# Performance work log

Measured on AMD Instinct MI355X. Metric: run time of the kernel, lower is better.

Reference implementation:

```python
import jax, jax.numpy as jnp
import numpy as np

SR = 22050
N_FFT = 16384
HOP = N_FFT // 2
NF = N_FFT // 2               # 8192 freq bins kept (last rfft bin dropped via [:-1])
H = SR / N_FFT                # uniform FFT-bin spacing in Hz
CENT = (440.0 * 2.0 ** ((np.arange(24, 108, 0.01) - 69.0) / 12.0)).astype(np.float32)  # [8400]
WIN = (0.5 - 0.5 * np.cos(2.0 * np.pi * np.arange(N_FFT) / N_FFT)).astype(np.float32)  # periodic hann

# Data-independent Thomas-algorithm coefficients for the not-a-knot cubic-spline
# tridiagonal system (diag=4, off-diags=1) with M_UNK unknowns (M_2..M_{n-3}).
M_UNK = NF - 4
_cp = np.empty(M_UNK); _inv_den = np.empty(M_UNK)
_inv_den[0] = 0.25; _cp[0] = 0.25
for _i in range(1, M_UNK):
    _inv_den[_i] = 1.0 / (4.0 - _cp[_i - 1])
    _cp[_i] = _inv_den[_i] if _i < M_UNK - 1 else 0.0
CP = jnp.asarray(_cp, jnp.float32)
INV_DEN = jnp.asarray(_inv_den, jnp.float32)
A_LOWER = jnp.asarray(np.where(np.arange(M_UNK) == 0, 0.0, 1.0), jnp.float32)


def _tridiag_solve(rhs):
    # Thomas algorithm with precomputed (data-independent) elimination coeffs.
    def fwd(dprev, xs):
        r, a, inv = xs
        dp = (r - a * dprev) * inv
        return dp, dp
    _, dp = jax.lax.scan(fwd, jnp.float32(0.0), (rhs, A_LOWER, INV_DEN))
    def bwd(xnext, xs):
        d_i, c_i = xs
        x = d_i - c_i * xnext
        return x, x
    _, xs = jax.lax.scan(bwd, jnp.float32(0.0), (dp, CP), reverse=True)
    return xs


def _cubic_interp(y, xq):
    # Not-a-knot cubic spline (scipy interp1d kind='cubic') on uniform grid x_i = i*H.
    h = jnp.float32(H)
    d = (y[:-2] - 2.0 * y[1:-1] + y[2:]) / (h * h)   # second-difference targets d_1..d_{n-2}
    M1, Mn2 = d[0], d[-1]                             # not-a-knot => M_1=d_1, M_{n-2}=d_{n-2}
    rhs = 6.0 * d[1:-1]
    rhs = rhs.at[0].add(-M1).at[-1].add(-Mn2)
    Min = _tridiag_solve(rhs)                         # M_2..M_{n-3}
    M = jnp.concatenate([jnp.stack([2.0 * M1 - Min[0], M1]), Min,
                         jnp.stack([Mn2, 2.0 * Mn2 - Min[-1]])])  # [n] second derivatives
    i = jnp.clip(jnp.floor(xq / h).astype(jnp.int32), 0, y.shape[0] - 2)
    t = xq - i.astype(jnp.float32) * h
    u = h - t
    Mi, Mi1, yi, yi1 = M[i], M[i + 1], y[i], y[i + 1]
    return ((Mi * u ** 3 + Mi1 * t ** 3) / (6.0 * h)
            + (yi - Mi * h * h / 6.0) * u / h
            + (yi1 - Mi1 * h * h / 6.0) * t / h)


def _tuning_scores(audio, w_smooth, w_detect):
    # torchaudio Spectrogram: center reflect-pad, periodic hann, power=2
    x = jnp.pad(audio, N_FFT // 2, mode='reflect')
    T = 1 + (x.shape[0] - N_FFT) // HOP
    idx = jnp.arange(T)[:, None] * HOP + jnp.arange(N_FFT)[None, :]
    frames = x[idx] * jnp.asarray(WIN)                 # [T, n_fft]
    spec = jnp.abs(jnp.fft.rfft(frames, axis=1)) ** 2  # [T, n_fft//2+1]
    fft_spec = jnp.log(100.0 * spec + 1.0).sum(0)[:NF] # sum over time, drop Nyquist bin
    cent = _cubic_interp(fft_spec, jnp.asarray(CENT))  # [8400]
    smoothed = jnp.convolve(cent, w_smooth, mode='same')
    filtered = jax.nn.relu(cent - smoothed)
    scores = jax.lax.conv_general_dilated(
        filtered[None, None, :], w_detect[None, None, :],
        window_strides=(1,), padding=[(50, 50)], rhs_dilation=(100,))[0, 0, :100]
    return scores


def setup_inputs():
    key = jax.random.key(0)
    audio = jax.random.normal(key, (16777216,), dtype=jnp.float32)
    w_smooth = jnp.ones((101,), jnp.float32) / 101.0   # mean filter, as in module init
    w_detect = jnp.ones((84,), jnp.float32)            # all-ones detector kernel
    return {"audio": audio, "w_smooth": w_smooth, "w_detect": w_detect}


def reference(audio, w_smooth, w_detect):
    scores = _tuning_scores(audio, w_smooth, w_detect)
    detuning = (jnp.argmax(scores) - 50).astype(jnp.int32)
    return detuning, scores
```

## Files before the change

### kernel.cpp

```cpp
#include <hip/hip_runtime.h>
#include <math.h>

#define NBINS   8192
#define L_AUDIO 16777216
#define T_FRAMES 2049
#define NQ      8400
#define MUNK    8188

__device__ __forceinline__ int refl_idx(int m) {
    if (m < 0) m = -m;
    if (m >= L_AUDIO) m = 2 * L_AUDIO - 2 - m;
    return m;
}
__device__ __forceinline__ float2 cmul(float2 a, float2 b) {
    return make_float2(fmaf(a.x, b.x, -a.y * b.y), fmaf(a.x, b.y, a.y * b.x));
}
__device__ __forceinline__ float2 csq(float2 a) {
    return make_float2(fmaf(a.x, a.x, -a.y * a.y), 2.0f * a.x * a.y);
}
__device__ __forceinline__ void r4(float2& x0, float2& x1, float2& x2, float2& x3,
                                   float2 w1, float2 w2, float2 w3) {
    float2 t0 = make_float2(x0.x + x2.x, x0.y + x2.y);
    float2 t1 = make_float2(x1.x + x3.x, x1.y + x3.y);
    float2 t2 = make_float2(x0.x - x2.x, x0.y - x2.y);
    float2 t3 = make_float2(x1.x - x3.x, x1.y - x3.y);
    float2 b1 = make_float2(t2.x + t3.y, t2.y - t3.x);
    float2 b3 = make_float2(t2.x - t3.y, t2.y + t3.x);
    x0 = make_float2(t0.x + t1.x, t0.y + t1.y);
    x1 = cmul(w1, b1);
    x2 = cmul(w2, make_float2(t0.x - t1.x, t0.y - t1.y));
    x3 = cmul(w3, b3);
}
__device__ __forceinline__ void r8(float2 x[8], float2 w) {
    const float c = 0.70710678118654752f;
    float2 w2 = csq(w), w3 = cmul(w, w2), w4 = csq(w2);
    r4(x[0], x[2], x[4], x[6], w, w2, w3);
    float2 wE   = make_float2(c * (w.x + w.y),  c * (w.y - w.x));
    float2 w2E2 = make_float2(w2.y, -w2.x);
    float2 w3E3 = make_float2(c * (w3.y - w3.x), -c * (w3.x + w3.y));
    r4(x[1], x[3], x[5], x[7], wE, w2E2, w3E3);
#pragma unroll
    for (int r = 0; r < 4; ++r) {
        float2 a = x[2 * r], b = x[2 * r + 1];
        x[2 * r]     = make_float2(a.x + b.x, a.y + b.y);
        float2 d     = make_float2(a.x - b.x, a.y - b.y);
        x[2 * r + 1] = cmul(w4, d);
    }
}

__global__ __launch_bounds__(512, 2) void fft_pow_kernel(
        const float* __restrict__ audio, float* __restrict__ partial, int P) {
    __shared__ float2 buf[8718];
    const int t = threadIdx.x;

    if (blockIdx.x == 0 && t == 0) {
        unsigned int* cz = (unsigned int*)(partial - 4);
        cz[0] = 0u;
    }

    const int phit  = t + (t >> 4);
    const int q2    = t & 127;
    const int base2 = 1090 * (t >> 7) + q2 + (q2 >> 4);
    const int base3 = 136 * (t >> 4) + ((t >> 4) >> 2) + (t & 15);
    const int base4 = 17 * t + (t >> 5);
    const int tp    = (512 - t) & 511;
    const int PBt = (t & 3) * 2048 + ((t >> 2) & 1) * 1024 + ((t >> 3) & 3) * 256
                  + ((t >> 5) & 1) * 128 + ((t >> 6) & 3) * 32 + ((t >> 8) & 1) * 16;
    const int PBp = (tp & 3) * 2048 + ((tp >> 2) & 1) * 1024 + ((tp >> 3) & 3) * 256
                  + ((tp >> 5) & 1) * 128 + ((tp >> 6) & 3) * 32 + ((tp >> 8) & 1) * 16;
    const int ubA = PBt + (PBt >> 4) + (PBt >> 9);
    const int ubB = PBp + (PBp >> 4) + (PBp >> 9);

    const float2 ONE = make_float2(1.0f, 0.0f);
    const float2 K8  = make_float2(0.92387953251128674f, -0.38268343236508977f);
    const float2 KD  = make_float2(0.99999992646574f, -0.00038349518757f);
    float2 wU  = make_float2(cospif((float)t * (1.0f / 8192.0f)),
                             -sinpif((float)t * (1.0f / 8192.0f)));
    float2 w1  = csq(wU);
    float2 wodd = cmul(w1, KD);
    float2 w2t = make_float2(cospif((float)q2 * (1.0f / 512.0f)),
                             -sinpif((float)q2 * (1.0f / 512.0f)));
    float2 w3t = make_float2(cospif((float)(t & 15) * (1.0f / 64.0f)),
                             -sinpif((float)(t & 15) * (1.0f / 64.0f)));
    const float K16c[16] = {1.0f, 0.98078528040323044f, 0.92387953251128674f,
        0.83146961230254524f, 0.70710678118654752f, 0.55557023301960222f,
        0.38268343236508977f, 0.19509032201612825f, 0.0f, -0.19509032201612825f,
        -0.38268343236508977f, -0.55557023301960222f, -0.70710678118654752f,
        -0.83146961230254524f, -0.92387953251128674f, -0.98078528040323044f};
    const float K16s[16] = {0.0f, -0.19509032201612825f, -0.38268343236508977f,
        -0.55557023301960222f, -0.70710678118654752f, -0.83146961230254524f,
        -0.92387953251128674f, -0.98078528040323044f, -1.0f, -0.98078528040323044f,
        -0.92387953251128674f, -0.83146961230254524f, -0.70710678118654752f,
        -0.55557023301960222f, -0.38268343236508977f, -0.19509032201612825f};
    const float W16C[16] = {1.0f, 0.92387953251128674f, 0.70710678118654752f,
        0.38268343236508977f, 0.0f, -0.38268343236508977f, -0.70710678118654752f,
        -0.92387953251128674f, -1.0f, -0.92387953251128674f, -0.70710678118654752f,
        -0.38268343236508977f, 0.0f, 0.38268343236508977f, 0.70710678118654752f,
        0.92387953251128674f};
    const float W16S[16] = {0.0f, 0.38268343236508977f, 0.70710678118654752f,
        0.92387953251128674f, 1.0f, 0.92387953251128674f, 0.70710678118654752f,
        0.38268343236508977f, 0.0f, -0.38268343236508977f, -0.70710678118654752f,
        -0.92387953251128674f, -1.0f, -0.92387953251128674f, -0.70710678118654752f,
        -0.38268343236508977f};

    float acc[16];
#pragma unroll
    for (int u = 0; u < 16; ++u) acc[u] = 0.0f;

    for (int f = blockIdx.x; f < T_FRAMES; f += P) {
        __syncthreads();
        const bool interior = (f != 0) && (f != T_FRAMES - 1);
        const float2* au2 = (const float2*)audio + 4096 * (f - 1);
        const int baseS = f * 8192 - 8192;
#pragma unroll 1
        for (int g = 0; g < 2; ++g) {
            float2 x[8];
            if (interior) {
#pragma unroll
                for (int j = 0; j < 8; ++j) {
                    int idx = t + 512 * g + 1024 * j;
                    float2 p = au2[idx];
                    const int uix = g + 2 * j;
                    float c0 = 0.5f - 0.5f * (w1.x * W16C[uix] + w1.y * W16S[uix]);
                    float c1 = 0.5f - 0.5f * (wodd.x * W16C[uix] + wodd.y * W16S[uix]);
                    x[j] = make_float2(p.x * c0, p.y * c1);
                }
            } else {
#pragma unroll
                for (int j = 0; j < 8; ++j) {
                    int idx = t + 512 * g + 1024 * j;
                    float a0 = audio[refl_idx(baseS + 2 * idx)];
                    float a1 = audio[refl_idx(baseS + 2 * idx + 1)];
                    const int uix = g + 2 * j;
                    float c0 = 0.5f - 0.5f * (w1.x * W16C[uix] + w1.y * W16S[uix]);
                    float c1 = 0.5f - 0.5f * (wodd.x * W16C[uix] + wodd.y * W16S[uix]);
                    x[j] = make_float2(a0 * c0, a1 * c1);
                }
            }
            float2 w = g ? cmul(w1, K8) : w1;
            r8(x, w);
#pragma unroll
            for (int j = 0; j < 8; ++j) buf[phit + 545 * g + 1090 * j] = x[j];
        }
        __syncthreads();
#pragma unroll 1
        for (int g = 0; g < 2; ++g) {
            float2 x[8];
            const int bs = base2 + 4360 * g;
#pragma unroll
            for (int j = 0; j < 8; ++j) x[j] = buf[bs + 136 * j + (j >> 2)];
            r8(x, w2t);
#pragma unroll
            for (int j = 0; j < 8; ++j) buf[bs + 136 * j + (j >> 2)] = x[j];
        }
        __syncthreads();
#pragma unroll 1
        for (int g = 0; g < 2; ++g) {
            float2 x[8];
            const int bs = base3 + 4360 * g;
#pragma unroll
            for (int j = 0; j < 8; ++j) x[j] = buf[bs + 17 * j];
            r8(x, w3t);
#pragma unroll
            for (int j = 0; j < 8; ++j) buf[bs + 17 * j] = x[j];
        }
        __syncthreads();
        {
            float2 a[8], x[8];
#pragma unroll
            for (int j = 0; j < 8; ++j) a[j] = buf[base4 + 2 * j];
            r8(a, ONE);
#pragma unroll
            for (int j = 0; j < 8; ++j) x[j] = buf[base4 + 1 + 2 * j];
            r8(x, K8);
#pragma unroll
            for (int j = 0; j < 8; ++j) {
                buf[base4 + 2 * j]     = make_float2(a[j].x + x[j].x, a[j].y + x[j].y);
                buf[base4 + 2 * j + 1] = make_float2(a[j].x - x[j].x, a[j].y - x[j].y);
            }
        }
        __syncthreads();
#pragma unroll
        for (int u = 0; u < 16; ++u) {
            const int off = (u & 3) * 4 + ((u >> 2) & 1) * 2 + (u >> 3);
            int u2 = t ? (15 - u) : ((16 - u) & 15);
            int off2 = (u2 & 3) * 4 + ((u2 >> 2) & 1) * 2 + (u2 >> 3);
            float2 A = buf[ubA + off];
            float2 B = buf[ubB + off2];
            float Xer = 0.5f * (A.x + B.x);
            float Xei = 0.5f * (A.y - B.y);
            float Xor = 0.5f * (A.y + B.y);
            float Xoi = -0.5f * (A.x - B.x);
            float2 w = cmul(wU, make_float2(K16c[u], K16s[u]));
            float Xr = Xer + Xor * w.x - Xoi * w.y;
            float Xi = Xei + Xor * w.y + Xoi * w.x;
            float pw = Xr * Xr + Xi * Xi;
            acc[u] += __logf(fmaf(100.0f, pw, 1.0f));
        }
    }
#pragma unroll
    for (int u = 0; u < 16; ++u)
        partial[(size_t)blockIdx.x * NBINS + t + 512 * u] = acc[u];
}

__global__ __launch_bounds__(128) void reduce_kernel(
        const float* __restrict__ partial, float* __restrict__ spec, int P) {
    __shared__ float4 s[4][33];
    const int bin0 = blockIdx.x * 128;
    const int co = threadIdx.x & 31;
    const int g  = threadIdx.x >> 5;
    const int rows = P >> 2;
    const int RS = NBINS / 4;
    const float4* base = (const float4*)(partial + (size_t)g * rows * NBINS + bin0) + co;
    float4 a0 = make_float4(0.f, 0.f, 0.f, 0.f);
    float4 a1 = make_float4(0.f, 0.f, 0.f, 0.f);
    int r = 0;
    for (; r + 16 <= rows; r += 16) {
        float4 l[16];
#pragma unroll
        for (int q = 0; q < 16; ++q) l[q] = base[(size_t)(r + q) * RS];
#pragma unroll
        for (int q = 0; q < 16; q += 2) {
            a0.x += l[q].x; a0.y += l[q].y; a0.z += l[q].z; a0.w += l[q].w;
            a1.x += l[q+1].x; a1.y += l[q+1].y; a1.z += l[q+1].z; a1.w += l[q+1].w;
        }
    }
    for (; r + 2 <= rows; r += 2) {
        float4 l0 = base[(size_t)r * RS];
        float4 l1 = base[(size_t)(r + 1) * RS];
        a0.x += l0.x; a0.y += l0.y; a0.z += l0.z; a0.w += l0.w;
        a1.x += l1.x; a1.y += l1.y; a1.z += l1.z; a1.w += l1.w;
    }
    for (; r < rows; ++r) {
        float4 l0 = base[(size_t)r * RS];
        a0.x += l0.x; a0.y += l0.y; a0.z += l0.z; a0.w += l0.w;
    }
    s[g][co] = make_float4(a0.x + a1.x, a0.y + a1.y, a0.z + a1.z, a0.w + a1.w);
    __syncthreads();
    if (threadIdx.x < 32) {
        float4 s0 = s[0][threadIdx.x], s1 = s[1][threadIdx.x];
        float4 s2 = s[2][threadIdx.x], s3 = s[3][threadIdx.x];
        float4 v = make_float4((s0.x + s1.x) + (s2.x + s3.x),
                               (s0.y + s1.y) + (s2.y + s3.y),
                               (s0.z + s1.z) + (s2.z + s3.z),
                               (s0.w + s1.w) + (s2.w + s3.w));
        if (!(blockIdx.x == 63 && threadIdx.x == 31))
            ((float4*)(spec + bin0))[threadIdx.x] = v;
    }
}

__global__ __launch_bounds__(256) void cent_spline_comb_kernel(
        const float* __restrict__ spec, const float* __restrict__ wsm,
        const float* __restrict__ wdet, float* __restrict__ filt,
        float* __restrict__ out) {
    __shared__ float ys[768];
    __shared__ float dps[704];
    __shared__ float Ms[640];
    __shared__ float cs[356];
    __shared__ float wsm_s[101];
    __shared__ float invden_s[64];
    const int tid = threadIdx.x;
    const int j0 = blockIdx.x * 256;
    const float h = 22050.0f / 16384.0f;
    const float hh = h * h;

    if (tid == 0) {
        double v = 0.25;
        invden_s[0] = 0.25f;
        for (int i = 1; i < 64; ++i) { v = 1.0 / (4.0 - v); invden_s[i] = (float)v; }
    }
    for (int r = tid; r < 101; r += 256) wsm_s[r] = wsm[r];

    const int jLo = max(j0 - 50, 0);
    const int jHi = min(j0 + 305, NQ - 1);
    const float xqLo = (float)(440.0 * exp2(((double)jLo * 0.01 - 45.0) * (1.0 / 12.0)));
    const float xqHi = (float)(440.0 * exp2(((double)jHi * 0.01 - 45.0) * (1.0 / 12.0)));
    const int iLo = min(max((int)floorf(xqLo / h), 0), 8190);
    const int iHi = min(max((int)floorf(xqHi / h), 0), 8190);
    const int pLo = max(iLo - 2, 0);
    const int pHi = min(iHi - 1, MUNK - 1);
    const int bHi = min(pHi + 64, MUNK - 1);
    const int yLo = max(pLo - 64, 0);
    const int yHi = bHi + 3;
    const int ny  = yHi - yLo + 1;

    for (int k = tid; k < ny; k += 256) ys[k] = spec[yLo + k];
    __syncthreads();
    const float cst = invden_s[63];

    {
        const int nch = (bHi - pLo + 32) >> 5;
        if (tid < nch) {
            const int s = pLo + (tid << 5);
            const int e = min(s + 31, bHi);
            const int ws = max(s - 64, 0);
            float dprev = 0.0f;
            for (int i = ws; i <= e; ++i) {
                float d1 = (ys[i + 1 - yLo] - 2.0f * ys[i + 2 - yLo]
                            + ys[i + 3 - yLo]) / hh;
                float r = 6.0f * d1;
                if (i == 0) r -= (ys[0] - 2.0f * ys[1] + ys[2]) / hh;
                float val = (i == 0) ? r : (r - dprev);
                float dpv = val * ((i < 64) ? invden_s[i] : cst);
                if (i >= s) dps[i - pLo] = dpv;
                dprev = dpv;
            }
        }
    }
    __syncthreads();
    {
        const int nch = (pHi - pLo + 32) >> 5;
        if (tid < nch) {
            const int s = pLo + (tid << 5);
            const int e = min(s + 31, pHi);
            const int ws2 = min(e + 64, bHi);
            float xnext = 0.0f;
            for (int i = ws2; i >= s; --i) {
                float cp = (i == MUNK - 1) ? 0.0f : ((i < 64) ? invden_s[i] : cst);
                float xv = dps[i - pLo] - cp * xnext;
                if (i <= e) Ms[2 + i - iLo] = xv;
                xnext = xv;
            }
        }
    }
    __syncthreads();
    for (int r = tid; r < 356; r += 256) {
        int j = j0 - 50 + r;
        float v = 0.0f;
        if (j >= 0 && j < NQ) {
            double e = ((double)j * 0.01 - 45.0) * (1.0 / 12.0);
            float xq = (float)(440.0 * exp2(e));
            int i = min(max((int)floorf(xq / h), 0), 8190);
            float tt = xq - (float)i * h;
            float uu = h - tt;
            float Mi = Ms[i - iLo], Mi1 = Ms[i + 1 - iLo];
            float yi = ys[i - yLo], yi1 = ys[i + 1 - yLo];
            v = (Mi * uu * uu * uu + Mi1 * tt * tt * tt) / (6.0f * h)
              + (yi - Mi * hh / 6.0f) * uu / h
              + (yi1 - Mi1 * hh / 6.0f) * tt / h;
        }
        cs[r] = v;
    }
    __syncthreads();
    int j = j0 + tid;
    if (j < NQ) {
        float s = 0.0f;
        for (int m = 0; m < 101; ++m) s = fmaf(wsm_s[m], cs[tid + 100 - m], s);
        float fv = cs[tid + 50] - s;
        filt[j] = fv > 0.0f ? fv : 0.0f;
    }
    __syncthreads();

    __shared__ unsigned int lastflag;
    unsigned int* cnt = (unsigned int*)(spec + 8188);
    __threadfence();
    if (tid == 0) {
        unsigned int prev =
            __hip_atomic_fetch_add(cnt, 1u, __ATOMIC_ACQ_REL, __HIP_MEMORY_SCOPE_AGENT);
        lastflag = (prev == 32u) ? 1u : 0u;
    }
    __syncthreads();
    if (!lastflag) return;
    __threadfence();

    {
        __shared__ float fs[NQ];
        __shared__ float wd[84];
        __shared__ float sc[100];
        const int t = tid;
        for (int k = t; k < NQ; k += 256) fs[k] = filt[k];
        if (t < 84) wd[t] = wdet[t];
        __syncthreads();
        if (t < 100) {
            float s = 0.0f;
            for (int k = 0; k < 84; ++k) {
                int ix = t - 50 + 100 * k;
                if (ix >= 0) s = fmaf(wd[k], fs[ix], s);
            }
            sc[t] = s;
            out[1 + t] = s;
        }
        __syncthreads();
        if (t < 64) {
            float v = (t < 100) ? sc[t] : -1e30f;
            int i = t;
            int t2 = t + 64;
            float v2 = (t2 < 100) ? sc[t2] : -1e30f;
            if (v2 > v) { v = v2; i = t2; }
#pragma unroll
            for (int off = 32; off; off >>= 1) {
                float ov = __shfl_xor(v, off, 64);
                int   oi = __shfl_xor(i, off, 64);
                if (ov > v || (ov == v && oi < i)) { v = ov; i = oi; }
            }
            if (t == 0) out[0] = (float)(i - 50);
        }
    }
}

extern "C" void kernel_launch(void* const* d_in, const int* in_sizes, int n_in,
                              void* d_out, int out_size, void* d_ws, size_t ws_size,
                              hipStream_t stream) {
    const float* audio = (const float*)d_in[0];
    const float* wsm   = (const float*)d_in[1];
    const float* wdet  = (const float*)d_in[2];
    float* out = (float*)d_out;
    float* ws  = (float*)d_ws;

    long cap = (long)(ws_size / sizeof(float) / NBINS) - 1;
    int P = (int)(cap < 4 ? 4 : (cap > 512 ? 512 : cap));
    P &= ~3;
    float* spec    = ws;
    float* partial = ws + NBINS;
    float* filt    = ws + 2 * NBINS;

    hipLaunchKernelGGL(fft_pow_kernel, dim3(P), dim3(512), 0, stream,
                       audio, partial, P);
    hipLaunchKernelGGL(reduce_kernel, dim3(64), dim3(128), 0, stream,
                       partial, spec, P);
    hipLaunchKernelGGL(cent_spline_comb_kernel, dim3(33), dim3(256), 0, stream,
                       spec, wsm, wdet, filt, out);
}
```

Measured before the change: 113.8 us.

## Split the leftover final frame FFT across two blocks and finish it in reduce

With 2049 frames spread over 512 blocks, one block had to process an extra full 16384-point frame on its own, which creates a serial tail. The main loop now stops at frame 2048. Blocks 0 and 1 then each compute a 4096-point half-size FFT of the even or odd samples of the last frame and write the results to workspace. The reduce kernel combines the two halves with a radix-2 step, does the real-FFT unpacking and adds the log-power into the spectrum. This roughly halves the tail work, at the cost of extra twiddle math and scattered reads in the reduce kernel, and it needs enough workspace to enable the split path.

```diff
diff --git a/kernel.cpp b/kernel.cpp
--- a/kernel.cpp
+++ b/kernel.cpp
@@ -47,9 +47,17 @@
         x[2 * r + 1] = cmul(w4, d);
     }
 }
+__device__ __forceinline__ int jof(int r) {
+    return ((r >> 1) & 1) * 4 + (r & 1) * 2 + (r >> 2);
+}
+__device__ __forceinline__ int posOf(int m) {
+    return 512 * jof(m & 7) + 64 * jof((m >> 3) & 7)
+         + 8 * jof((m >> 6) & 7) + jof(m >> 9);
+}
 
 __global__ __launch_bounds__(512, 2) void fft_pow_kernel(
-        const float* __restrict__ audio, float* __restrict__ partial, int P) {
+        const float* __restrict__ audio, float* __restrict__ partial, int P,
+        int fmax, float* __restrict__ Fout) {
     __shared__ float2 buf[8718];
     const int t = threadIdx.x;
 
@@ -107,7 +115,7 @@
 #pragma unroll
     for (int u = 0; u < 16; ++u) acc[u] = 0.0f;
 
-    for (int f = blockIdx.x; f < T_FRAMES; f += P) {
+    for (int f = blockIdx.x; f < fmax; f += P) {
         __syncthreads();
         const bool interior = (f != 0) && (f != T_FRAMES - 1);
         const float2* au2 = (const float2*)audio + 4096 * (f - 1);
@@ -201,10 +209,82 @@
 #pragma unroll
     for (int u = 0; u < 16; ++u)
         partial[(size_t)blockIdx.x * NBINS + t + 512 * u] = acc[u];
+
+    if (Fout != (float*)0 && blockIdx.x < 2) {
+        const int r = blockIdx.x;
+        __syncthreads();
+        const int baseS = 2048 * 8192 - 8192;
+        float2 wr = make_float2(cospif((float)(4 * t + 2 * r) * (1.0f / 8192.0f)),
+                                -sinpif((float)(4 * t + 2 * r) * (1.0f / 8192.0f)));
+        float2 wro = cmul(wr, KD);
+        const int phit2 = t + (t >> 4);
+        {
+            float2 x[8];
+#pragma unroll
+            for (int j = 0; j < 8; ++j) {
+                int m = t + 512 * j;
+                int s0 = baseS + 4 * m + 2 * r;
+                float a0 = audio[refl_idx(s0)];
+                float a1 = audio[refl_idx(s0 + 1)];
+                float c0 = 0.5f - 0.5f * (wr.x * W16C[2 * j] + wr.y * W16S[2 * j]);
+                float c1 = 0.5f - 0.5f * (wro.x * W16C[2 * j] + wro.y * W16S[2 * j]);
+                x[j] = make_float2(a0 * c0, a1 * c1);
+            }
+            float2 w = make_float2(cospif((float)t * (1.0f / 2048.0f)),
+                                   -sinpif((float)t * (1.0f / 2048.0f)));
+            r8(x, w);
+#pragma unroll
+            for (int j = 0; j < 8; ++j) buf[phit2 + 544 * j] = x[j];
+        }
+        __syncthreads();
+        {
+            const int q = t & 63;
+            const int bs = 544 * (t >> 6) + q + (q >> 4);
+            float2 x[8];
+#pragma unroll
+            for (int j = 0; j < 8; ++j) x[j] = buf[bs + 68 * j];
+            float2 w = make_float2(cospif((float)q * (1.0f / 256.0f)),
+                                   -sinpif((float)q * (1.0f / 256.0f)));
+            r8(x, w);
+#pragma unroll
+            for (int j = 0; j < 8; ++j) buf[bs + 68 * j] = x[j];
+        }
+        __syncthreads();
+        {
+            const int q = t & 7;
+            const int bs = 68 * (t >> 3) + q;
+            const int OF3[8] = {0, 8, 17, 25, 34, 42, 51, 59};
+            float2 x[8];
+#pragma unroll
+            for (int j = 0; j < 8; ++j) x[j] = buf[bs + OF3[j]];
+            float2 w = make_float2(cospif((float)q * (1.0f / 32.0f)),
+                                   -sinpif((float)q * (1.0f / 32.0f)));
+            r8(x, w);
+#pragma unroll
+            for (int j = 0; j < 8; ++j) buf[bs + OF3[j]] = x[j];
+        }
+        __syncthreads();
+        {
+            const int bs = 8 * t + (t >> 1);
+            float2 x[8];
+#pragma unroll
+            for (int j = 0; j < 8; ++j) x[j] = buf[bs + j];
+            r8(x, ONE);
+#pragma unroll
+            for (int j = 0; j < 8; ++j) buf[bs + j] = x[j];
+        }
+        __syncthreads();
+        {
+            float2* fo = (float2*)Fout + r * 4096;
+#pragma unroll
+            for (int j = 0; j < 8; ++j) fo[t + 512 * j] = buf[phit2 + 544 * j];
+        }
+    }
 }
 
 __global__ __launch_bounds__(128) void reduce_kernel(
-        const float* __restrict__ partial, float* __restrict__ spec, int P) {
+        const float* __restrict__ partial, float* __restrict__ spec, int P,
+        const float* __restrict__ F) {
     __shared__ float4 s[4][33];
     const int bin0 = blockIdx.x * 128;
     const int co = threadIdx.x & 31;
@@ -244,6 +324,38 @@
                                (s0.y + s1.y) + (s2.y + s3.y),
                                (s0.z + s1.z) + (s2.z + s3.z),
                                (s0.w + s1.w) + (s2.w + s3.w));
+        if (F != (const float*)0) {
+            const float2* F0 = (const float2*)F;
+            const float2* F1 = F0 + 4096;
+            float* vv = &v.x;
+#pragma unroll
+            for (int c = 0; c < 4; ++c) {
+                int b = bin0 + 4 * threadIdx.x + c;
+                int kh = b & 4095;
+                float2 E = F0[posOf(kh)], O = F1[posOf(kh)];
+                float2 wk = make_float2(cospif((float)b * (1.0f / 4096.0f)),
+                                        -sinpif((float)b * (1.0f / 4096.0f)));
+                float2 Xk = make_float2(E.x + wk.x * O.x - wk.y * O.y,
+                                        E.y + wk.x * O.y + wk.y * O.x);
+                int pb = (8192 - b) & 8191;
+                int ph = pb & 4095;
+                float2 Ep = F0[posOf(ph)], Op = F1[posOf(ph)];
+                float2 wp = make_float2(cospif((float)pb * (1.0f / 4096.0f)),
+                                        -sinpif((float)pb * (1.0f / 4096.0f)));
+                float2 Xp = make_float2(Ep.x + wp.x * Op.x - wp.y * Op.y,
+                                        Ep.y + wp.x * Op.y + wp.y * Op.x);
+                float Xer = 0.5f * (Xk.x + Xp.x);
+                float Xei = 0.5f * (Xk.y - Xp.y);
+                float Xor = 0.5f * (Xk.y + Xp.y);
+                float Xoi = -0.5f * (Xk.x - Xp.x);
+                float2 wu = make_float2(cospif((float)b * (1.0f / 8192.0f)),
+                                        -sinpif((float)b * (1.0f / 8192.0f)));
+                float Xr = Xer + Xor * wu.x - Xoi * wu.y;
+                float Xi = Xei + Xor * wu.y + Xoi * wu.x;
+                float pw = Xr * Xr + Xi * Xi;
+                vv[c] += __logf(fmaf(100.0f, pw, 1.0f));
+            }
+        }
         if (!(blockIdx.x == 63 && threadIdx.x == 31))
             ((float4*)(spec + bin0))[threadIdx.x] = v;
     }
@@ -414,10 +526,14 @@
     float* partial = ws + NBINS;
     float* filt    = ws + 2 * NBINS;
 
+    int doSplit = (P == 512 && cap >= (long)P + 3) ? 1 : 0;
+    float* F = doSplit ? (ws + (size_t)(1 + P) * NBINS) : (float*)0;
+    int fmax = doSplit ? 2048 : T_FRAMES;
+
     hipLaunchKernelGGL(fft_pow_kernel, dim3(P), dim3(512), 0, stream,
-                       audio, partial, P);
+                       audio, partial, P, fmax, F);
     hipLaunchKernelGGL(reduce_kernel, dim3(64), dim3(128), 0, stream,
-                       partial, spec, P);
+                       partial, spec, P, F);
     hipLaunchKernelGGL(cent_spline_comb_kernel, dim3(33), dim3(256), 0, stream,
                        spec, wsm, wdet, filt, out);
 }
```

New measurement: 111.8 us. About the same (-1.8%).
